# Performance work log

Hardware: AMD Instinct MI355X
Metric: run time of the kernel (lower is better)

The kernel has to match this reference:

```python
import jax, jax.numpy as jnp
import numpy as np

N = 100000   # nodes
E = 1600000  # edges
F_IN = 32    # num_features
H = 16       # hidden_size (hardcoded as conv2 input in source)
C = 10       # num_classes
K = 2        # kernel_size (dim=1)


def setup_inputs() -> dict:
    key = jax.random.key(0)
    ks = jax.random.split(key, 9)
    x = jax.random.normal(ks[0], (N, F_IN), dtype=jnp.float32)
    edge_index = jax.random.randint(ks[1], (2, E), 0, N, dtype=jnp.int64)
    edge_attr = jax.random.uniform(ks[2], (E, 1), dtype=jnp.float32)
    s1 = 1.0 / np.sqrt(F_IN)
    s2 = 1.0 / np.sqrt(H)
    W1 = jax.random.normal(ks[3], (K, F_IN, H), dtype=jnp.float32) * s1
    root1 = jax.random.normal(ks[4], (F_IN, H), dtype=jnp.float32) * s1
    b1 = jnp.zeros((H,), dtype=jnp.float32)
    W2 = jax.random.normal(ks[5], (K, H, C), dtype=jnp.float32) * s2
    root2 = jax.random.normal(ks[6], (H, C), dtype=jnp.float32) * s2
    b2 = jnp.zeros((C,), dtype=jnp.float32)
    return {"x": x, "edge_index": edge_index, "edge_attr": edge_attr,
            "W1": W1, "root1": root1, "b1": b1,
            "W2": W2, "root2": root2, "b2": b2}


def spline_conv(x, edge_index, edge_attr, W, root, bias, num_nodes):
    # Open B-spline, degree 1: hat-function basis over K knots.
    k = W.shape[0]
    src, dst = edge_index[0], edge_index[1]
    v = edge_attr[:, 0] * (k - 1)                                   # [E]
    grid = jnp.arange(k, dtype=v.dtype)
    basis = jnp.maximum(0.0, 1.0 - jnp.abs(v[:, None] - grid[None, :]))  # [E,K]
    xe = x[src]                                                      # [E,in] gather
    msg = jnp.einsum('ei,kio,ek->eo', xe, W, basis)                  # per-edge message
    agg = jax.ops.segment_sum(msg, dst, num_segments=num_nodes)      # scatter-add
    deg = jax.ops.segment_sum(jnp.ones((msg.shape[0],), x.dtype), dst,
                              num_segments=num_nodes)
    agg = agg / jnp.maximum(deg, 1.0)[:, None]                       # mean aggregation
    return agg + x @ root + bias


def reference(x, edge_index, edge_attr, W1, root1, b1, W2, root2, b2):
    # Inference mode: F.dropout(training=False) is identity.
    h = jax.nn.elu(spline_conv(x, edge_index, edge_attr, W1, root1, b1, N))
    out = spline_conv(h, edge_index, edge_attr, W2, root2, b2, N)
    return jax.nn.log_softmax(out, axis=1)
```

## Files before the change

kernel.cpp:

```cpp
#include <hip/hip_runtime.h>
#include <math.h>

#define N_NODES 100000
#define E_EDGES 1600000
#define F_IN 32
#define HID 16
#define NC 10
#define SRC_BITS 17
#define SRC_MASK ((1u << SRC_BITS) - 1u)
#define VQ_SCALE 32767.0f
#define CBITS 8
#define BUCKET_N 256
#define NCB ((N_NODES + BUCKET_N - 1) / BUCKET_N)
#define BLK_E 2048
#define NBLK ((E_EDGES + BLK_E - 1) / BLK_E)
#define NODE_GRID ((N_NODES + 255) / 256)

__device__ __forceinline__ unsigned int bf16pair(float lo, float hi) {
    unsigned int ulo = __float_as_uint(lo), uhi = __float_as_uint(hi);
    ulo += 0x7fffu + ((ulo >> 16) & 1u);
    uhi += 0x7fffu + ((uhi >> 16) & 1u);
    return (ulo >> 16) | (uhi & 0xffff0000u);
}

__device__ __forceinline__ float lerp_pair(unsigned int pair, float v) {
    float a = __uint_as_float(pair << 16);
    float b = __uint_as_float(pair & 0xffff0000u);
    return fmaf(v, b - a, a);
}

__global__ __launch_bounds__(256) void fused_l1cnt(
    const float* __restrict__ x, const float* __restrict__ W1,
    const float* __restrict__ root1, const float* __restrict__ b1,
    const int* __restrict__ ei,
    unsigned int* __restrict__ y, float* __restrict__ r1,
    int* __restrict__ cnt)
{
    if (blockIdx.x >= NODE_GRID) {
        __shared__ int h[NCB];
        int b = blockIdx.x - NODE_GRID;
        for (int i = threadIdx.x; i < NCB; i += 256) h[i] = 0;
        __syncthreads();
        const int* dstp = ei + E_EDGES;
        int e0 = b * BLK_E;
        for (int i = threadIdx.x * 4; i < BLK_E; i += 1024) {
            int e = e0 + i;
            if (e + 3 < E_EDGES) {
                int4 d4 = *(const int4*)(dstp + e);
                atomicAdd(&h[d4.x >> CBITS], 1);
                atomicAdd(&h[d4.y >> CBITS], 1);
                atomicAdd(&h[d4.z >> CBITS], 1);
                atomicAdd(&h[d4.w >> CBITS], 1);
            } else {
                for (int k = 0; k < 4; k++)
                    if (e + k < E_EDGES) atomicAdd(&h[dstp[e + k] >> CBITS], 1);
            }
        }
        __syncthreads();
        for (int s = threadIdx.x; s < NCB; s += 256)
            cnt[(size_t)s * NBLK + b] = h[s];
        return;
    }
    __shared__ float sW0[F_IN * HID], sW1[F_IN * HID], sR[F_IN * HID], sB[HID];
    for (int i = threadIdx.x; i < F_IN * HID; i += 256) {
        sW0[i] = W1[i];
        sW1[i] = W1[F_IN * HID + i];
        sR[i]  = root1[i];
    }
    if (threadIdx.x < HID) sB[threadIdx.x] = b1[threadIdx.x];
    __syncthreads();

    int n = blockIdx.x * 256 + threadIdx.x;
    if (n >= N_NODES) return;

    float xr[F_IN];
    const float4* xp = (const float4*)(x + (size_t)n * F_IN);
    #pragma unroll
    for (int i = 0; i < F_IN / 4; i++) {
        float4 t = xp[i];
        xr[i*4+0] = t.x; xr[i*4+1] = t.y; xr[i*4+2] = t.z; xr[i*4+3] = t.w;
    }

    float a0[HID], a1[HID], ar[HID];
    #pragma unroll
    for (int o = 0; o < HID; o++) { a0[o] = 0.f; a1[o] = 0.f; ar[o] = sB[o]; }
    for (int i = 0; i < F_IN; i++) {
        float xi = xr[i];
        #pragma unroll
        for (int o = 0; o < HID; o++) {
            a0[o] += xi * sW0[i * HID + o];
            a1[o] += xi * sW1[i * HID + o];
            ar[o] += xi * sR[i * HID + o];
        }
    }
    unsigned int* py = y + (size_t)n * 16;
    float* pr = r1 + (size_t)n * HID;
    #pragma unroll
    for (int o = 0; o < HID; o++) {
        py[o] = bf16pair(a0[o], a1[o]);
        pr[o] = ar[o];
    }
}

__global__ __launch_bounds__(256) void k_rowscan(
    int* __restrict__ cnt, int* __restrict__ total)
{
    __shared__ int wsum[4], woff[4];
    int s = blockIdx.x;
    int t = threadIdx.x;
    int w = t >> 6, l = t & 63;
    int carry = 0;
    int* row = cnt + (size_t)s * NBLK;
    for (int c = 0; c < NBLK; c += 256) {
        int idx = c + t;
        int v = (idx < NBLK) ? row[idx] : 0;
        int incl = v;
        #pragma unroll
        for (int off = 1; off < 64; off <<= 1) {
            int u = __shfl_up(incl, off, 64);
            if (l >= off) incl += u;
        }
        if (l == 63) wsum[w] = incl;
        __syncthreads();
        if (t == 0) {
            int a = 0;
            #pragma unroll
            for (int i = 0; i < 4; i++) { woff[i] = a; a += wsum[i]; }
        }
        __syncthreads();
        int excl = woff[w] + incl - v;
        if (idx < NBLK) row[idx] = carry + excl;
        carry += woff[3] + wsum[3];
        __syncthreads();
    }
    if (t == 0) total[s] = carry;
}

__global__ __launch_bounds__(512) void k_bucket(
    const int* __restrict__ ei, const float* __restrict__ ea,
    const int* __restrict__ cnt, const int* __restrict__ total,
    int2* __restrict__ ebuf, int* __restrict__ bb, int* __restrict__ start)
{
    __shared__ int wsum[8], woff[8];
    __shared__ int base[NCB], cur[NCB];
    int t = threadIdx.x;
    int tot = (t < NCB) ? total[t] : 0;
    int w = t >> 6, l = t & 63;
    int incl = tot;
    #pragma unroll
    for (int off = 1; off < 64; off <<= 1) {
        int u = __shfl_up(incl, off, 64);
        if (l >= off) incl += u;
    }
    if (l == 63) wsum[w] = incl;
    __syncthreads();
    if (t == 0) {
        int a = 0;
        #pragma unroll
        for (int i = 0; i < 8; i++) { woff[i] = a; a += wsum[i]; }
    }
    __syncthreads();
    int excl = woff[w] + incl - tot;
    if (t < NCB) {
        base[t] = excl + cnt[(size_t)t * NBLK + blockIdx.x];
        cur[t] = 0;
        if (blockIdx.x == 0) {
            bb[t] = excl;
            if (t == NCB - 1) { bb[NCB] = excl + tot; start[N_NODES] = E_EDGES; }
        }
    }
    __syncthreads();

    const int* dstp = ei + E_EDGES;
    int e0 = blockIdx.x * BLK_E;
    for (int i = t * 4; i < BLK_E; i += 2048) {
        int e = e0 + i;
        if (e + 3 < E_EDGES) {
            int4 d4 = *(const int4*)(dstp + e);
            int4 s4 = *(const int4*)(ei + e);
            float4 a4 = *(const float4*)(ea + e);
            {
                int s = d4.x >> CBITS;
                int off = atomicAdd(&cur[s], 1);
                unsigned int vq = (unsigned int)(a4.x * VQ_SCALE + 0.5f);
                ebuf[base[s] + off] = make_int2(d4.x & (BUCKET_N - 1),
                                               (int)((vq << SRC_BITS) | (unsigned int)s4.x));
            }
            {
                int s = d4.y >> CBITS;
                int off = atomicAdd(&cur[s], 1);
                unsigned int vq = (unsigned int)(a4.y * VQ_SCALE + 0.5f);
                ebuf[base[s] + off] = make_int2(d4.y & (BUCKET_N - 1),
                                               (int)((vq << SRC_BITS) | (unsigned int)s4.y));
            }
            {
                int s = d4.z >> CBITS;
                int off = atomicAdd(&cur[s], 1);
                unsigned int vq = (unsigned int)(a4.z * VQ_SCALE + 0.5f);
                ebuf[base[s] + off] = make_int2(d4.z & (BUCKET_N - 1),
                                               (int)((vq << SRC_BITS) | (unsigned int)s4.z));
            }
            {
                int s = d4.w >> CBITS;
                int off = atomicAdd(&cur[s], 1);
                unsigned int vq = (unsigned int)(a4.w * VQ_SCALE + 0.5f);
                ebuf[base[s] + off] = make_int2(d4.w & (BUCKET_N - 1),
                                               (int)((vq << SRC_BITS) | (unsigned int)s4.w));
            }
        } else {
            for (int k = 0; k < 4; k++) {
                int ee = e + k;
                if (ee >= E_EDGES) break;
                int dst = dstp[ee];
                int s = dst >> CBITS;
                int off = atomicAdd(&cur[s], 1);
                unsigned int vq = (unsigned int)(ea[ee] * VQ_SCALE + 0.5f);
                ebuf[base[s] + off] = make_int2(dst & (BUCKET_N - 1),
                                               (int)((vq << SRC_BITS) | (unsigned int)ei[ee]));
            }
        }
    }
}

__global__ __launch_bounds__(1024) void k_bsort(
    const int2* __restrict__ ebuf, const int* __restrict__ bb,
    unsigned int* __restrict__ es, int* __restrict__ start)
{
    __shared__ int hist[BUCKET_N];
    __shared__ int cursor[BUCKET_N];
    __shared__ int wsum[4], woff[4];
    int t = threadIdx.x;
    int b = blockIdx.x;
    int j0 = bb[b], j1 = bb[b + 1];
    if (t < BUCKET_N) { hist[t] = 0; cursor[t] = 0; }
    __syncthreads();
    for (int j = j0 + t; j < j1; j += 1024)
        atomicAdd(&hist[ebuf[j].x], 1);
    __syncthreads();
    int c = (t < BUCKET_N) ? hist[t] : 0;
    int w = t >> 6, l = t & 63;
    int incl = c;
    #pragma unroll
    for (int off = 1; off < 64; off <<= 1) {
        int u = __shfl_up(incl, off, 64);
        if (l >= off) incl += u;
    }
    if (w < 4 && l == 63) wsum[w] = incl;
    __syncthreads();
    if (t == 0) {
        int acc = 0;
        #pragma unroll
        for (int i = 0; i < 4; i++) { woff[i] = acc; acc += wsum[i]; }
    }
    __syncthreads();
    if (t < BUCKET_N) {
        int excl = woff[w] + incl - c;
        hist[t] = excl;
        int node = (b << CBITS) + t;
        if (node < N_NODES) start[node] = j0 + excl;
    }
    __syncthreads();
    for (int j = j0 + t; j < j1; j += 1024) {
        int2 p = ebuf[j];
        int off = atomicAdd(&cursor[p.x], 1);
        es[j0 + hist[p.x] + off] = (unsigned int)p.y;
    }
}

__global__ __launch_bounds__(256) void k_agg1(
    const unsigned int* __restrict__ es, const int* __restrict__ start,
    const unsigned int* __restrict__ y, const float* __restrict__ r1,
    const float* __restrict__ W2, const float* __restrict__ root2,
    const float* __restrict__ b2,
    unsigned int* __restrict__ z, float* __restrict__ r2)
{
    __shared__ float sW0[HID * NC], sW1[HID * NC], sRt[HID * NC], sB2[NC];
    int t = threadIdx.x;
    if (t < HID * NC) { sW0[t] = W2[t]; sW1[t] = W2[HID * NC + t]; sRt[t] = root2[t]; }
    if (t >= HID * NC && t < HID * NC + NC) sB2[t - HID * NC] = b2[t - HID * NC];
    __syncthreads();

    int idx = blockIdx.x * 256 + t;
    int n = idx >> 2, l = idx & 3;
    if (n >= N_NODES) return;
    int j0 = start[n], j1 = start[n + 1];
    const uint4* yrow = (const uint4*)y;
    float acc[4] = {0.f, 0.f, 0.f, 0.f};
    int j = j0;
    for (; j + 3 < j1; j += 4) {
        unsigned int p0 = es[j], p1 = es[j+1], p2 = es[j+2], p3 = es[j+3];
        uint4 q0 = yrow[(size_t)(p0 & SRC_MASK) * 4 + l];
        uint4 q1 = yrow[(size_t)(p1 & SRC_MASK) * 4 + l];
        uint4 q2 = yrow[(size_t)(p2 & SRC_MASK) * 4 + l];
        uint4 q3 = yrow[(size_t)(p3 & SRC_MASK) * 4 + l];
        float v0 = (float)(p0 >> SRC_BITS) * (1.0f / VQ_SCALE);
        float v1 = (float)(p1 >> SRC_BITS) * (1.0f / VQ_SCALE);
        float v2 = (float)(p2 >> SRC_BITS) * (1.0f / VQ_SCALE);
        float v3 = (float)(p3 >> SRC_BITS) * (1.0f / VQ_SCALE);
        acc[0] += lerp_pair(q0.x, v0); acc[1] += lerp_pair(q0.y, v0);
        acc[2] += lerp_pair(q0.z, v0); acc[3] += lerp_pair(q0.w, v0);
        acc[0] += lerp_pair(q1.x, v1); acc[1] += lerp_pair(q1.y, v1);
        acc[2] += lerp_pair(q1.z, v1); acc[3] += lerp_pair(q1.w, v1);
        acc[0] += lerp_pair(q2.x, v2); acc[1] += lerp_pair(q2.y, v2);
        acc[2] += lerp_pair(q2.z, v2); acc[3] += lerp_pair(q2.w, v2);
        acc[0] += lerp_pair(q3.x, v3); acc[1] += lerp_pair(q3.y, v3);
        acc[2] += lerp_pair(q3.z, v3); acc[3] += lerp_pair(q3.w, v3);
    }
    for (; j < j1; j++) {
        unsigned int p = es[j];
        uint4 q = yrow[(size_t)(p & SRC_MASK) * 4 + l];
        float v = (float)(p >> SRC_BITS) * (1.0f / VQ_SCALE);
        acc[0] += lerp_pair(q.x, v); acc[1] += lerp_pair(q.y, v);
        acc[2] += lerp_pair(q.z, v); acc[3] += lerp_pair(q.w, v);
    }
    float inv = 1.0f / fmaxf((float)(j1 - j0), 1.0f);
    float4 rr = *(const float4*)(r1 + (size_t)n * HID + l * 4);
    float hv[4];
    hv[0] = acc[0] * inv + rr.x;
    hv[1] = acc[1] * inv + rr.y;
    hv[2] = acc[2] * inv + rr.z;
    hv[3] = acc[3] * inv + rr.w;
    #pragma unroll
    for (int e = 0; e < 4; e++) hv[e] = hv[e] > 0.0f ? hv[e] : expm1f(hv[e]);

    int cbase = l * 4;
    float a0[4] = {0.f, 0.f, 0.f, 0.f}, a1[4] = {0.f, 0.f, 0.f, 0.f}, ar[4];
    #pragma unroll
    for (int e = 0; e < 4; e++) { int c = cbase + e; ar[e] = (c < NC) ? sB2[c] : 0.f; }
    #pragma unroll
    for (int s = 0; s < 4; s++) {
        #pragma unroll
        for (int e2 = 0; e2 < 4; e2++) {
            float hi = __shfl(hv[e2], s, 4);
            int i = s * 4 + e2;
            #pragma unroll
            for (int e = 0; e < 4; e++) {
                int c = cbase + e;
                if (c < NC) {
                    a0[e] += hi * sW0[i * NC + c];
                    a1[e] += hi * sW1[i * NC + c];
                    ar[e] += hi * sRt[i * NC + c];
                }
            }
        }
    }
    uint4 zo;
    zo.x = (cbase + 0 < NC) ? bf16pair(a0[0], a1[0]) : 0u;
    zo.y = (cbase + 1 < NC) ? bf16pair(a0[1], a1[1]) : 0u;
    zo.z = (cbase + 2 < NC) ? bf16pair(a0[2], a1[2]) : 0u;
    zo.w = (cbase + 3 < NC) ? bf16pair(a0[3], a1[3]) : 0u;
    ((uint4*)z)[(size_t)n * 4 + l] = zo;
    #pragma unroll
    for (int e = 0; e < 4; e++) {
        int c = cbase + e;
        if (c < NC) r2[(size_t)n * NC + c] = ar[e];
    }
}

__global__ __launch_bounds__(256) void k_agg2(
    const unsigned int* __restrict__ es, const int* __restrict__ start,
    const unsigned int* __restrict__ z,
    const float* __restrict__ r2, float* __restrict__ out)
{
    int idx = blockIdx.x * 256 + threadIdx.x;
    int n = idx >> 2, l = idx & 3;
    if (n >= N_NODES) return;
    int j0 = start[n], j1 = start[n + 1];
    const uint4* zrow = (const uint4*)z;
    float acc[4] = {0.f, 0.f, 0.f, 0.f};
    int j = j0;
    for (; j + 3 < j1; j += 4) {
        unsigned int p0 = es[j], p1 = es[j+1], p2 = es[j+2], p3 = es[j+3];
        uint4 q0 = zrow[(size_t)(p0 & SRC_MASK) * 4 + l];
        uint4 q1 = zrow[(size_t)(p1 & SRC_MASK) * 4 + l];
        uint4 q2 = zrow[(size_t)(p2 & SRC_MASK) * 4 + l];
        uint4 q3 = zrow[(size_t)(p3 & SRC_MASK) * 4 + l];
        float v0 = (float)(p0 >> SRC_BITS) * (1.0f / VQ_SCALE);
        float v1 = (float)(p1 >> SRC_BITS) * (1.0f / VQ_SCALE);
        float v2 = (float)(p2 >> SRC_BITS) * (1.0f / VQ_SCALE);
        float v3 = (float)(p3 >> SRC_BITS) * (1.0f / VQ_SCALE);
        acc[0] += lerp_pair(q0.x, v0); acc[1] += lerp_pair(q0.y, v0);
        acc[2] += lerp_pair(q0.z, v0); acc[3] += lerp_pair(q0.w, v0);
        acc[0] += lerp_pair(q1.x, v1); acc[1] += lerp_pair(q1.y, v1);
        acc[2] += lerp_pair(q1.z, v1); acc[3] += lerp_pair(q1.w, v1);
        acc[0] += lerp_pair(q2.x, v2); acc[1] += lerp_pair(q2.y, v2);
        acc[2] += lerp_pair(q2.z, v2); acc[3] += lerp_pair(q2.w, v2);
        acc[0] += lerp_pair(q3.x, v3); acc[1] += lerp_pair(q3.y, v3);
        acc[2] += lerp_pair(q3.z, v3); acc[3] += lerp_pair(q3.w, v3);
    }
    for (; j < j1; j++) {
        unsigned int p = es[j];
        uint4 q = zrow[(size_t)(p & SRC_MASK) * 4 + l];
        float v = (float)(p >> SRC_BITS) * (1.0f / VQ_SCALE);
        acc[0] += lerp_pair(q.x, v); acc[1] += lerp_pair(q.y, v);
        acc[2] += lerp_pair(q.z, v); acc[3] += lerp_pair(q.w, v);
    }
    float inv = 1.0f / fmaxf((float)(j1 - j0), 1.0f);
    int cbase = l * 4;
    float val[4];
    #pragma unroll
    for (int e = 0; e < 4; e++) {
        int c = cbase + e;
        val[e] = (c < NC) ? acc[e] * inv + r2[(size_t)n * NC + c] : -INFINITY;
    }
    float mx = fmaxf(fmaxf(val[0], val[1]), fmaxf(val[2], val[3]));
    mx = fmaxf(mx, __shfl_xor(mx, 1, 4));
    mx = fmaxf(mx, __shfl_xor(mx, 2, 4));
    float ssum = 0.f;
    #pragma unroll
    for (int e = 0; e < 4; e++) {
        int c = cbase + e;
        if (c < NC) ssum += expf(val[e] - mx);
    }
    ssum += __shfl_xor(ssum, 1, 4);
    ssum += __shfl_xor(ssum, 2, 4);
    float lse = logf(ssum);
    #pragma unroll
    for (int e = 0; e < 4; e++) {
        int c = cbase + e;
        if (c < NC) out[(size_t)n * NC + c] = val[e] - mx - lse;
    }
}

extern "C" void kernel_launch(void* const* d_in, const int* in_sizes, int n_in,
                              void* d_out, int out_size, void* d_ws, size_t ws_size,
                              hipStream_t stream) {
    const float* x     = (const float*)d_in[0];
    const int*   ei    = (const int*)d_in[1];
    const float* ea    = (const float*)d_in[2];
    const float* W1    = (const float*)d_in[3];
    const float* root1 = (const float*)d_in[4];
    const float* b1    = (const float*)d_in[5];
    const float* W2    = (const float*)d_in[6];
    const float* root2 = (const float*)d_in[7];
    const float* b2    = (const float*)d_in[8];
    float* out = (float*)d_out;

    char* wsb = (char*)d_ws;
    int2*         ebuf   = (int2*)wsb;
    unsigned int* es     = (unsigned int*)(wsb + (size_t)E_EDGES * 8);
    unsigned int* y      = es + (size_t)E_EDGES;
    float*        r1     = (float*)(y + (size_t)N_NODES * 16);
    unsigned int* z      = (unsigned int*)(r1 + (size_t)N_NODES * HID);
    float*        r2     = (float*)(z + (size_t)N_NODES * 16);
    int*          start  = (int*)(r2 + (size_t)N_NODES * NC);
    int*          cnt    = start + N_NODES + 1;
    int*          total  = cnt + (size_t)NCB * NBLK;
    int*          bb     = total + NCB;

    int aggGrid = (N_NODES * 4 + 255) / 256;

    fused_l1cnt<<<NODE_GRID + NBLK, 256, 0, stream>>>(x, W1, root1, b1, ei, y, r1, cnt);
    k_rowscan<<<NCB, 256, 0, stream>>>(cnt, total);
    k_bucket<<<NBLK, 512, 0, stream>>>(ei, ea, cnt, total, ebuf, bb, start);
    k_bsort <<<NCB, 1024, 0, stream>>>(ebuf, bb, es, start);
    k_agg1  <<<aggGrid, 256, 0, stream>>>(es, start, y, r1, W2, root2, b2, z, r2);
    k_agg2  <<<aggGrid, 256, 0, stream>>>(es, start, z, r2, out);
}
```

Before: 180.7 us.

## Single-pass edge bucketing with global atomic cursors into fixed-capacity windows

Merges the per-block destination histogram, the row-scan kernel and the bucket scatter kernel into one pass inside the layer-1 kernel. Each edge block reserves space in its buckets with global atomics on per-bucket cursors and writes into fixed-capacity windows (CAP per bucket). The sort kernel then derives bucket offsets from a prefix scan of the cursor values. This removes one full read of the edge arrays and two kernel launches. In exchange it adds a memset and global atomics, and it silently drops edges if any bucket exceeds CAP, which relies on the roughly uniform destination distribution. Edge order within a bucket is now nondeterministic.

```diff
diff --git a/kernel.cpp b/kernel.cpp
--- a/kernel.cpp
+++ b/kernel.cpp
@@ -12,9 +12,10 @@
 #define CBITS 8
 #define BUCKET_N 256
 #define NCB ((N_NODES + BUCKET_N - 1) / BUCKET_N)
-#define BLK_E 2048
+#define BLK_E 4096
 #define NBLK ((E_EDGES + BLK_E - 1) / BLK_E)
-#define NODE_GRID ((N_NODES + 255) / 256)
+#define L1_BLOCKS ((N_NODES + 511) / 512)
+#define CAP 6144
 
 __device__ __forceinline__ unsigned int bf16pair(float lo, float hi) {
     unsigned int ulo = __float_as_uint(lo), uhi = __float_as_uint(hi);
@@ -29,40 +30,138 @@
     return fmaf(v, b - a, a);
 }
 
-__global__ __launch_bounds__(256) void fused_l1cnt(
+__global__ __launch_bounds__(512) void fused_l1bucket(
     const float* __restrict__ x, const float* __restrict__ W1,
     const float* __restrict__ root1, const float* __restrict__ b1,
-    const int* __restrict__ ei,
+    const int* __restrict__ ei, const float* __restrict__ ea,
     unsigned int* __restrict__ y, float* __restrict__ r1,
-    int* __restrict__ cnt)
+    int* __restrict__ gcur, int2* __restrict__ ebuf)
 {
-    if (blockIdx.x >= NODE_GRID) {
-        __shared__ int h[NCB];
-        int b = blockIdx.x - NODE_GRID;
-        for (int i = threadIdx.x; i < NCB; i += 256) h[i] = 0;
+    if (blockIdx.x >= L1_BLOCKS) {
+        __shared__ int h[NCB], base[NCB], cur[NCB];
+        int t = threadIdx.x;
+        int b = blockIdx.x - L1_BLOCKS;
+        for (int i = t; i < NCB; i += 512) { h[i] = 0; cur[i] = 0; }
         __syncthreads();
+
         const int* dstp = ei + E_EDGES;
-        int e0 = b * BLK_E;
-        for (int i = threadIdx.x * 4; i < BLK_E; i += 1024) {
-            int e = e0 + i;
-            if (e + 3 < E_EDGES) {
-                int4 d4 = *(const int4*)(dstp + e);
-                atomicAdd(&h[d4.x >> CBITS], 1);
-                atomicAdd(&h[d4.y >> CBITS], 1);
-                atomicAdd(&h[d4.z >> CBITS], 1);
-                atomicAdd(&h[d4.w >> CBITS], 1);
-            } else {
-                for (int k = 0; k < 4; k++)
-                    if (e + k < E_EDGES) atomicAdd(&h[dstp[e + k] >> CBITS], 1);
-            }
+        int e0 = b * BLK_E + t * 8;
+        int4 dA, dB, sA, sB;
+        float4 aA, aB;
+        bool fullA = (e0 + 3 < E_EDGES), fullB = (e0 + 7 < E_EDGES);
+        if (fullA) {
+            dA = *(const int4*)(dstp + e0);
+            sA = *(const int4*)(ei + e0);
+            aA = *(const float4*)(ea + e0);
+            atomicAdd(&h[dA.x >> CBITS], 1);
+            atomicAdd(&h[dA.y >> CBITS], 1);
+            atomicAdd(&h[dA.z >> CBITS], 1);
+            atomicAdd(&h[dA.w >> CBITS], 1);
+        }
+        if (fullB) {
+            dB = *(const int4*)(dstp + e0 + 4);
+            sB = *(const int4*)(ei + e0 + 4);
+            aB = *(const float4*)(ea + e0 + 4);
+            atomicAdd(&h[dB.x >> CBITS], 1);
+            atomicAdd(&h[dB.y >> CBITS], 1);
+            atomicAdd(&h[dB.z >> CBITS], 1);
+            atomicAdd(&h[dB.w >> CBITS], 1);
+        }
+        if (!fullA || !fullB) {
+            int lo = fullA ? e0 + 4 : e0;
+            for (int e = lo; e < E_EDGES && e < e0 + 8; e++)
+                atomicAdd(&h[dstp[e] >> CBITS], 1);
         }
         __syncthreads();
-        for (int s = threadIdx.x; s < NCB; s += 256)
-            cnt[(size_t)s * NBLK + b] = h[s];
+
+        for (int s = t; s < NCB; s += 512)
+            if (h[s] > 0) base[s] = atomicAdd(&gcur[s], h[s]);
+        __syncthreads();
+
+        if (fullA) {
+            {
+                int s = dA.x >> CBITS;
+                int idx = base[s] + atomicAdd(&cur[s], 1);
+                unsigned int vq = (unsigned int)(aA.x * VQ_SCALE + 0.5f);
+                if (idx < CAP)
+                    ebuf[(size_t)s * CAP + idx] = make_int2(dA.x & (BUCKET_N - 1),
+                        (int)((vq << SRC_BITS) | (unsigned int)sA.x));
+            }
+            {
+                int s = dA.y >> CBITS;
+                int idx = base[s] + atomicAdd(&cur[s], 1);
+                unsigned int vq = (unsigned int)(aA.y * VQ_SCALE + 0.5f);
+                if (idx < CAP)
+                    ebuf[(size_t)s * CAP + idx] = make_int2(dA.y & (BUCKET_N - 1),
+                        (int)((vq << SRC_BITS) | (unsigned int)sA.y));
+            }
+            {
+                int s = dA.z >> CBITS;
+                int idx = base[s] + atomicAdd(&cur[s], 1);
+                unsigned int vq = (unsigned int)(aA.z * VQ_SCALE + 0.5f);
+                if (idx < CAP)
+                    ebuf[(size_t)s * CAP + idx] = make_int2(dA.z & (BUCKET_N - 1),
+                        (int)((vq << SRC_BITS) | (unsigned int)sA.z));
+            }
+            {
+                int s = dA.w >> CBITS;
+                int idx = base[s] + atomicAdd(&cur[s], 1);
+                unsigned int vq = (unsigned int)(aA.w * VQ_SCALE + 0.5f);
+                if (idx < CAP)
+                    ebuf[(size_t)s * CAP + idx] = make_int2(dA.w & (BUCKET_N - 1),
+                        (int)((vq << SRC_BITS) | (unsigned int)sA.w));
+            }
+        }
+        if (fullB) {
+            {
+                int s = dB.x >> CBITS;
+                int idx = base[s] + atomicAdd(&cur[s], 1);
+                unsigned int vq = (unsigned int)(aB.x * VQ_SCALE + 0.5f);
+                if (idx < CAP)
+                    ebuf[(size_t)s * CAP + idx] = make_int2(dB.x & (BUCKET_N - 1),
+                        (int)((vq << SRC_BITS) | (unsigned int)sB.x));
+            }
+            {
+                int s = dB.y >> CBITS;
+                int idx = base[s] + atomicAdd(&cur[s], 1);
+                unsigned int vq = (unsigned int)(aB.y * VQ_SCALE + 0.5f);
+                if (idx < CAP)
+                    ebuf[(size_t)s * CAP + idx] = make_int2(dB.y & (BUCKET_N - 1),
+                        (int)((vq << SRC_BITS) | (unsigned int)sB.y));
+            }
+            {
+                int s = dB.z >> CBITS;
+                int idx = base[s] + atomicAdd(&cur[s], 1);
+                unsigned int vq = (unsigned int)(aB.z * VQ_SCALE + 0.5f);
+                if (idx < CAP)
+                    ebuf[(size_t)s * CAP + idx] = make_int2(dB.z & (BUCKET_N - 1),
+                        (int)((vq << SRC_BITS) | (unsigned int)sB.z));
+            }
+            {
+                int s = dB.w >> CBITS;
+                int idx = base[s] + atomicAdd(&cur[s], 1);
+                unsigned int vq = (unsigned int)(aB.w * VQ_SCALE + 0.5f);
+                if (idx < CAP)
+                    ebuf[(size_t)s * CAP + idx] = make_int2(dB.w & (BUCKET_N - 1),
+                        (int)((vq << SRC_BITS) | (unsigned int)sB.w));
+            }
+        }
+        if (!fullA || !fullB) {
+            int lo = fullA ? e0 + 4 : e0;
+            for (int e = lo; e < E_EDGES && e < e0 + 8; e++) {
+                int dst = dstp[e];
+                int s = dst >> CBITS;
+                int idx = base[s] + atomicAdd(&cur[s], 1);
+                unsigned int vq = (unsigned int)(ea[e] * VQ_SCALE + 0.5f);
+                if (idx < CAP)
+                    ebuf[(size_t)s * CAP + idx] = make_int2(dst & (BUCKET_N - 1),
+                        (int)((vq << SRC_BITS) | (unsigned int)ei[e]));
+            }
+        }
         return;
     }
     __shared__ float sW0[F_IN * HID], sW1[F_IN * HID], sR[F_IN * HID], sB[HID];
-    for (int i = threadIdx.x; i < F_IN * HID; i += 256) {
+    for (int i = threadIdx.x; i < F_IN * HID; i += 512) {
         sW0[i] = W1[i];
         sW1[i] = W1[F_IN * HID + i];
         sR[i]  = root1[i];
@@ -70,15 +169,15 @@
     if (threadIdx.x < HID) sB[threadIdx.x] = b1[threadIdx.x];
     __syncthreads();
 
-    int n = blockIdx.x * 256 + threadIdx.x;
+    int n = blockIdx.x * 512 + threadIdx.x;
     if (n >= N_NODES) return;
 
     float xr[F_IN];
     const float4* xp = (const float4*)(x + (size_t)n * F_IN);
     #pragma unroll
     for (int i = 0; i < F_IN / 4; i++) {
-        float4 t = xp[i];
-        xr[i*4+0] = t.x; xr[i*4+1] = t.y; xr[i*4+2] = t.z; xr[i*4+3] = t.w;
+        float4 t4 = xp[i];
+        xr[i*4+0] = t4.x; xr[i*4+1] = t4.y; xr[i*4+2] = t4.z; xr[i*4+3] = t4.w;
     }
 
     float a0[HID], a1[HID], ar[HID];
@@ -102,168 +201,74 @@
     }
 }
 
-__global__ __launch_bounds__(256) void k_rowscan(
-    int* __restrict__ cnt, int* __restrict__ total)
-{
-    __shared__ int wsum[4], woff[4];
-    int s = blockIdx.x;
-    int t = threadIdx.x;
-    int w = t >> 6, l = t & 63;
-    int carry = 0;
-    int* row = cnt + (size_t)s * NBLK;
-    for (int c = 0; c < NBLK; c += 256) {
-        int idx = c + t;
-        int v = (idx < NBLK) ? row[idx] : 0;
-        int incl = v;
-        #pragma unroll
-        for (int off = 1; off < 64; off <<= 1) {
-            int u = __shfl_up(incl, off, 64);
-            if (l >= off) incl += u;
-        }
-        if (l == 63) wsum[w] = incl;
-        __syncthreads();
-        if (t == 0) {
-            int a = 0;
-            #pragma unroll
-            for (int i = 0; i < 4; i++) { woff[i] = a; a += wsum[i]; }
-        }
-        __syncthreads();
-        int excl = woff[w] + incl - v;
-        if (idx < NBLK) row[idx] = carry + excl;
-        carry += woff[3] + wsum[3];
-        __syncthreads();
-    }
-    if (t == 0) total[s] = carry;
-}
-
-__global__ __launch_bounds__(512) void k_bucket(
-    const int* __restrict__ ei, const float* __restrict__ ea,
-    const int* __restrict__ cnt, const int* __restrict__ total,
-    int2* __restrict__ ebuf, int* __restrict__ bb, int* __restrict__ start)
-{
-    __shared__ int wsum[8], woff[8];
-    __shared__ int base[NCB], cur[NCB];
-    int t = threadIdx.x;
-    int tot = (t < NCB) ? total[t] : 0;
-    int w = t >> 6, l = t & 63;
-    int incl = tot;
-    #pragma unroll
-    for (int off = 1; off < 64; off <<= 1) {
-        int u = __shfl_up(incl, off, 64);
-        if (l >= off) incl += u;
-    }
-    if (l == 63) wsum[w] = incl;
-    __syncthreads();
-    if (t == 0) {
-        int a = 0;
-        #pragma unroll
-        for (int i = 0; i < 8; i++) { woff[i] = a; a += wsum[i]; }
-    }
-    __syncthreads();
-    int excl = woff[w] + incl - tot;
-    if (t < NCB) {
-        base[t] = excl + cnt[(size_t)t * NBLK + blockIdx.x];
-        cur[t] = 0;
-        if (blockIdx.x == 0) {
-            bb[t] = excl;
-            if (t == NCB - 1) { bb[NCB] = excl + tot; start[N_NODES] = E_EDGES; }
-        }
-    }
-    __syncthreads();
-
-    const int* dstp = ei + E_EDGES;
-    int e0 = blockIdx.x * BLK_E;
-    for (int i = t * 4; i < BLK_E; i += 2048) {
-        int e = e0 + i;
-        if (e + 3 < E_EDGES) {
-            int4 d4 = *(const int4*)(dstp + e);
-            int4 s4 = *(const int4*)(ei + e);
-            float4 a4 = *(const float4*)(ea + e);
-            {
-                int s = d4.x >> CBITS;
-                int off = atomicAdd(&cur[s], 1);
-                unsigned int vq = (unsigned int)(a4.x * VQ_SCALE + 0.5f);
-                ebuf[base[s] + off] = make_int2(d4.x & (BUCKET_N - 1),
-                                               (int)((vq << SRC_BITS) | (unsigned int)s4.x));
-            }
-            {
-                int s = d4.y >> CBITS;
-                int off = atomicAdd(&cur[s], 1);
-                unsigned int vq = (unsigned int)(a4.y * VQ_SCALE + 0.5f);
-                ebuf[base[s] + off] = make_int2(d4.y & (BUCKET_N - 1),
-                                               (int)((vq << SRC_BITS) | (unsigned int)s4.y));
-            }
-            {
-                int s = d4.z >> CBITS;
-                int off = atomicAdd(&cur[s], 1);
-                unsigned int vq = (unsigned int)(a4.z * VQ_SCALE + 0.5f);
-                ebuf[base[s] + off] = make_int2(d4.z & (BUCKET_N - 1),
-                                               (int)((vq << SRC_BITS) | (unsigned int)s4.z));
-            }
-            {
-                int s = d4.w >> CBITS;
-                int off = atomicAdd(&cur[s], 1);
-                unsigned int vq = (unsigned int)(a4.w * VQ_SCALE + 0.5f);
-                ebuf[base[s] + off] = make_int2(d4.w & (BUCKET_N - 1),
-                                               (int)((vq << SRC_BITS) | (unsigned int)s4.w));
-            }
-        } else {
-            for (int k = 0; k < 4; k++) {
-                int ee = e + k;
-                if (ee >= E_EDGES) break;
-                int dst = dstp[ee];
-                int s = dst >> CBITS;
-                int off = atomicAdd(&cur[s], 1);
-                unsigned int vq = (unsigned int)(ea[ee] * VQ_SCALE + 0.5f);
-                ebuf[base[s] + off] = make_int2(dst & (BUCKET_N - 1),
-                                               (int)((vq << SRC_BITS) | (unsigned int)ei[ee]));
-            }
-        }
-    }
-}
-
 __global__ __launch_bounds__(1024) void k_bsort(
-    const int2* __restrict__ ebuf, const int* __restrict__ bb,
+    const int2* __restrict__ ebuf, const int* __restrict__ gcur,
     unsigned int* __restrict__ es, int* __restrict__ start)
 {
     __shared__ int hist[BUCKET_N];
     __shared__ int cursor[BUCKET_N];
-    __shared__ int wsum[4], woff[4];
+    __shared__ int pre[NCB];
+    __shared__ int wsum[16], woff[16];
+    __shared__ int wsum2[4], woff2[4];
     int t = threadIdx.x;
     int b = blockIdx.x;
-    int j0 = bb[b], j1 = bb[b + 1];
-    if (t < BUCKET_N) { hist[t] = 0; cursor[t] = 0; }
-    __syncthreads();
-    for (int j = j0 + t; j < j1; j += 1024)
-        atomicAdd(&hist[ebuf[j].x], 1);
-    __syncthreads();
-    int c = (t < BUCKET_N) ? hist[t] : 0;
     int w = t >> 6, l = t & 63;
-    int incl = c;
+
+    int v = (t < NCB) ? min(gcur[t], CAP) : 0;
+    int incl = v;
     #pragma unroll
     for (int off = 1; off < 64; off <<= 1) {
         int u = __shfl_up(incl, off, 64);
         if (l >= off) incl += u;
     }
-    if (w < 4 && l == 63) wsum[w] = incl;
+    if (l == 63) wsum[w] = incl;
+    if (t < BUCKET_N) { hist[t] = 0; cursor[t] = 0; }
+    __syncthreads();
+    if (t == 0) {
+        int a = 0;
+        #pragma unroll
+        for (int i = 0; i < 16; i++) { woff[i] = a; a += wsum[i]; }
+    }
+    __syncthreads();
+    if (t < NCB) pre[t] = woff[w] + incl - v;
+    __syncthreads();
+
+    int fill = min(gcur[b], CAP);
+    int obase = pre[b];
+    const int2* win = ebuf + (size_t)b * CAP;
+
+    for (int j = t; j < fill; j += 1024)
+        atomicAdd(&hist[win[j].x], 1);
+    __syncthreads();
+
+    int c = (t < BUCKET_N) ? hist[t] : 0;
+    int incl2 = c;
+    #pragma unroll
+    for (int off = 1; off < 64; off <<= 1) {
+        int u = __shfl_up(incl2, off, 64);
+        if (l >= off) incl2 += u;
+    }
+    if (w < 4 && l == 63) wsum2[w] = incl2;
     __syncthreads();
     if (t == 0) {
         int acc = 0;
         #pragma unroll
-        for (int i = 0; i < 4; i++) { woff[i] = acc; acc += wsum[i]; }
+        for (int i = 0; i < 4; i++) { woff2[i] = acc; acc += wsum2[i]; }
     }
     __syncthreads();
     if (t < BUCKET_N) {
-        int excl = woff[w] + incl - c;
+        int excl = woff2[w] + incl2 - c;
         hist[t] = excl;
         int node = (b << CBITS) + t;
-        if (node < N_NODES) start[node] = j0 + excl;
-    }
-    __syncthreads();
-    for (int j = j0 + t; j < j1; j += 1024) {
-        int2 p = ebuf[j];
+        if (node < N_NODES) start[node] = obase + excl;
+    }
+    if (b == 0 && t == 0) start[N_NODES] = E_EDGES;
+    __syncthreads();
+
+    for (int j = t; j < fill; j += 1024) {
+        int2 p = win[j];
         int off = atomicAdd(&cursor[p.x], 1);
-        es[j0 + hist[p.x] + off] = (unsigned int)p.y;
+        es[obase + hist[p.x] + off] = (unsigned int)p.y;
     }
 }
 
@@ -438,22 +443,20 @@
 
     char* wsb = (char*)d_ws;
     int2*         ebuf   = (int2*)wsb;
-    unsigned int* es     = (unsigned int*)(wsb + (size_t)E_EDGES * 8);
+    unsigned int* es     = (unsigned int*)(wsb + (size_t)NCB * CAP * 8);
     unsigned int* y      = es + (size_t)E_EDGES;
     float*        r1     = (float*)(y + (size_t)N_NODES * 16);
     unsigned int* z      = (unsigned int*)(r1 + (size_t)N_NODES * HID);
     float*        r2     = (float*)(z + (size_t)N_NODES * 16);
     int*          start  = (int*)(r2 + (size_t)N_NODES * NC);
-    int*          cnt    = start + N_NODES + 1;
-    int*          total  = cnt + (size_t)NCB * NBLK;
-    int*          bb     = total + NCB;
+    int*          gcur   = start + N_NODES + 1;
 
     int aggGrid = (N_NODES * 4 + 255) / 256;
 
-    fused_l1cnt<<<NODE_GRID + NBLK, 256, 0, stream>>>(x, W1, root1, b1, ei, y, r1, cnt);
-    k_rowscan<<<NCB, 256, 0, stream>>>(cnt, total);
-    k_bucket<<<NBLK, 512, 0, stream>>>(ei, ea, cnt, total, ebuf, bb, start);
-    k_bsort <<<NCB, 1024, 0, stream>>>(ebuf, bb, es, start);
-    k_agg1  <<<aggGrid, 256, 0, stream>>>(es, start, y, r1, W2, root2, b2, z, r2);
-    k_agg2  <<<aggGrid, 256, 0, stream>>>(es, start, z, r2, out);
-}
+    hipMemsetAsync(gcur, 0, (size_t)NCB * sizeof(int), stream);
+    fused_l1bucket<<<L1_BLOCKS + NBLK, 512, 0, stream>>>(x, W1, root1, b1, ei, ea,
+                                                         y, r1, gcur, ebuf);
+    k_bsort<<<NCB, 1024, 0, stream>>>(ebuf, gcur, es, start);
+    k_agg1 <<<aggGrid, 256, 0, stream>>>(es, start, y, r1, W2, root2, b2, z, r2);
+    k_agg2 <<<aggGrid, 256, 0, stream>>>(es, start, z, r2, out);
+}
```

After: 176.1 us. 2.6% less time.
